# Optimization experiments

Hardware: AMD Instinct MI355X
Metric: run time of the kernel (lower is better)

## Reference

```python
import jax, jax.numpy as jnp
import numpy as np

DIM = 256
NUM_HEADS = 4
HEAD_DIM = DIM // NUM_HEADS
SCALE = HEAD_DIM ** -0.5
LN_EPS = 1e-5


def setup_inputs() -> dict:
    key = jax.random.key(0)
    ks = jax.random.split(key, 12)
    V, B, C, H, W = 3, 2, DIM, 32, 32
    s = 0.02
    return {
        "features": jax.random.normal(ks[0], (V, B, C, H, W), jnp.float32),
        "Wq": jax.random.normal(ks[1], (DIM, DIM), jnp.float32) * s,
        "bq": jnp.zeros((DIM,), jnp.float32),
        "Wk": jax.random.normal(ks[2], (DIM, DIM), jnp.float32) * s,
        "bk": jnp.zeros((DIM,), jnp.float32),
        "Wv": jax.random.normal(ks[3], (DIM, DIM), jnp.float32) * s,
        "bv": jnp.zeros((DIM,), jnp.float32),
        "Wp": jax.random.normal(ks[4], (DIM, DIM), jnp.float32) * s,
        "bp": jnp.zeros((DIM,), jnp.float32),
        "gamma": jnp.ones((DIM,), jnp.float32),
        "beta": jnp.zeros((DIM,), jnp.float32),
    }


def reference(features, Wq, bq, Wk, bk, Wv, bv, Wp, bp, gamma, beta):
    V, B, C, H, W = features.shape
    N = H * W
    L = V * N
    # concat views along token axis: [B, V*N, C]
    x = features.reshape(V, B, C, N).transpose(1, 0, 3, 2).reshape(B, L, C)
    # QKV projections (torch Linear: x @ W.T + b)
    q = (x @ Wq.T + bq).reshape(B, L, NUM_HEADS, HEAD_DIM).transpose(0, 2, 1, 3)
    k = (x @ Wk.T + bk).reshape(B, L, NUM_HEADS, HEAD_DIM).transpose(0, 2, 1, 3)
    v = (x @ Wv.T + bv).reshape(B, L, NUM_HEADS, HEAD_DIM).transpose(0, 2, 1, 3)
    # full attention (chunked loop in original is exact, dropout off in eval)
    attn = jax.nn.softmax(jnp.einsum('bhqd,bhkd->bhqk', q, k) * SCALE, axis=-1)
    o = jnp.einsum('bhqk,bhkd->bhqd', attn, v)  # [B, H, L, D]
    o = o.transpose(0, 2, 1, 3).reshape(B, L, C)
    # output proj + LayerNorm
    o = o @ Wp.T + bp
    mu = jnp.mean(o, axis=-1, keepdims=True)
    var = jnp.mean(jnp.square(o - mu), axis=-1, keepdims=True)
    o = (o - mu) * jax.lax.rsqrt(var + LN_EPS) * gamma + beta
    # mean over views, back to [B, C, H, W]
    o = o.reshape(B, V, N, C).mean(axis=1)
    return o.reshape(B, H, W, C).transpose(0, 3, 1, 2)
```

## Files before the change

### kernel.cpp

```cpp
#include <hip/hip_runtime.h>
#include <hip/hip_bf16.h>

#define V_ 3
#define B_ 2
#define C_ 256
#define N_ 1024
#define L_ 3072
#define NH 4
#define DH 64
#define SCALE 0.125f
#define LOG2E 1.44269504088896340736f

typedef __attribute__((ext_vector_type(8))) short short8;
typedef __attribute__((ext_vector_type(4))) float floatx4;
typedef unsigned short u16;
typedef unsigned int u32;

__device__ __forceinline__ u16 f2bf(float f) {
    union { float f; u32 u; } c; c.f = f;
    u32 u = c.u;
    u32 lsb = (u >> 16) & 1u;
    u += 0x7fffu + lsb;
    return (u16)(u >> 16);
}
__device__ __forceinline__ u32 pk_bf16(float a, float b) {
    __hip_bfloat162 h = __float22bfloat162_rn(make_float2(a, b));
    union { __hip_bfloat162 h; u32 u; } cv; cv.h = h; return cv.u;
}

__global__ __launch_bounds__(256) void k_prep_gather(
    const float* __restrict__ feat,
    const float* __restrict__ Wq, const float* __restrict__ Wk,
    const float* __restrict__ Wv, const float* __restrict__ Wp,
    u16* __restrict__ x, u16* __restrict__ Wb) {
    int bid = blockIdx.x;
    int t = threadIdx.x;
    if (bid < 384) {
        __shared__ u16 tile[64][66];
        int n0 = (bid & 15) << 6;
        int c0 = ((bid >> 4) & 3) << 6;
        int b  = (bid >> 6) & 1;
        int v  = bid >> 7;
        const float* src = feat + ((size_t)((v * B_ + b) * C_ + c0)) * N_ + n0;
        for (int i = 0; i < 8; ++i) {
            int idx = i * 256 + t;
            int cl = idx >> 5;
            int np2 = idx & 31;
            float2 f = *(const float2*)(src + (size_t)cl * N_ + np2 * 2);
            *(u32*)&tile[cl][np2 * 2] = pk_bf16(f.x, f.y);
        }
        __syncthreads();
        u16* dst = x + ((size_t)(b * L_ + v * N_ + n0)) * C_ + c0;
        for (int i = 0; i < 8; ++i) {
            int idx = i * 256 + t;
            int nl = idx >> 5;
            int cl = (idx & 31) * 2;
            u32 uu = (u32)tile[cl][nl] | ((u32)tile[cl + 1][nl] << 16);
            *(u32*)(dst + (size_t)nl * C_ + cl) = uu;
        }
    } else {
        int idx = (bid - 384) * 256 + t;
        int g0 = idx * 16;
        int m = g0 >> 16;
        const float* src = (m == 0) ? Wq : (m == 1) ? Wk : (m == 2) ? Wv : Wp;
        int off = g0 & 65535;
#pragma unroll
        for (int e = 0; e < 8; ++e) {
            float2 f = *(const float2*)(src + off + e * 2);
            ((u32*)(Wb + g0))[e] = pk_bf16(f.x, f.y);
        }
    }
}

__global__ __launch_bounds__(64) void k_qkv(
    const u16* __restrict__ x, const u16* __restrict__ Wb,
    const float* __restrict__ bq, const float* __restrict__ bk,
    const float* __restrict__ bv,
    u16* __restrict__ Qf, u16* __restrict__ Kf, u16* __restrict__ Vf) {
    int bid = blockIdx.x;
    int npc = bid & 3;
    int rest = bid >> 2;
    int m  = rest / 192;
    int rb = rest % 192;
    int b  = rb / 96;
    int r0 = (rb % 96) * 32;
    int lane = threadIdx.x;
    int quad = lane >> 4, m16 = lane & 15;

    const u16* xrow0 = x + ((size_t)(b * L_ + r0 + m16)) * C_ + quad * 8;
    const u16* xrow1 = xrow0 + (size_t)16 * C_;
    short8 a0[8], a1[8];
#pragma unroll
    for (int kc = 0; kc < 8; ++kc) {
        a0[kc] = *(const short8*)(xrow0 + kc * 32);
        a1[kc] = *(const short8*)(xrow1 + kc * 32);
    }
    const u16* W = Wb + (size_t)m * 65536;

    if (m == 2) {
#pragma unroll
        for (int np = npc * 2; np < npc * 2 + 2; ++np) {
            int nt0 = np * 2;
            const u16* w0 = W + (size_t)(nt0 * 16 + m16) * C_ + quad * 8;
            const u16* w1 = w0 + 16 * C_;
            short8 wf0[8], wf1[8];
#pragma unroll
            for (int kc = 0; kc < 8; ++kc) {
                wf0[kc] = *(const short8*)(w0 + kc * 32);
                wf1[kc] = *(const short8*)(w1 + kc * 32);
            }
            floatx4 acc00 = {0.f,0.f,0.f,0.f}, acc01 = {0.f,0.f,0.f,0.f};
            floatx4 acc10 = {0.f,0.f,0.f,0.f}, acc11 = {0.f,0.f,0.f,0.f};
#pragma unroll
            for (int kc = 0; kc < 8; ++kc) {
                acc00 = __builtin_amdgcn_mfma_f32_16x16x32_bf16(a0[kc], wf0[kc], acc00, 0, 0, 0);
                acc01 = __builtin_amdgcn_mfma_f32_16x16x32_bf16(a0[kc], wf1[kc], acc01, 0, 0, 0);
                acc10 = __builtin_amdgcn_mfma_f32_16x16x32_bf16(a1[kc], wf0[kc], acc10, 0, 0, 0);
                acc11 = __builtin_amdgcn_mfma_f32_16x16x32_bf16(a1[kc], wf1[kc], acc11, 0, 0, 0);
            }
#pragma unroll
            for (int gi = 0; gi < 2; ++gi)
#pragma unroll
            for (int half = 0; half < 2; ++half) {
                int dout = (nt0 + half) * 16 + m16;
                float bias = bv[dout];
                int h = dout >> 6, dh = dout & 63;
                size_t bh = (size_t)(b * NH + h);
                floatx4 acc = gi ? (half ? acc11 : acc10) : (half ? acc01 : acc00);
                float f0 = acc[0] + bias, f1 = acc[1] + bias;
                float f2 = acc[2] + bias, f3 = acc[3] + bias;
                int lr0 = r0 + gi * 16 + quad * 4;
                int tile = lr0 >> 6, kk = lr0 & 63;
                int halfv = kk >> 5, quadp = (kk >> 3) & 3, j0 = kk & 7;
                int ntv = dh >> 4, m16pp = dh & 15;
                u32* p = (u32*)(Vf + (bh * 48 + tile) * 4096 +
                                ((size_t)((ntv * 2 + halfv) * 64 + quadp * 16 + m16pp)) * 8 + j0);
                p[0] = pk_bf16(f0, f1);
                p[1] = pk_bf16(f2, f3);
            }
        }
    } else {
        const float* bs = (m == 0) ? bq : bk;
        float scale = (m == 0) ? (SCALE * LOG2E) : 1.0f;
#pragma unroll
        for (int np = npc * 2; np < npc * 2 + 2; ++np) {
            int nt0 = np * 2;
            const u16* w0 = W + (size_t)(nt0 * 16 + m16) * C_ + quad * 8;
            const u16* w1 = w0 + 16 * C_;
            short8 wf0[8], wf1[8];
#pragma unroll
            for (int kc = 0; kc < 8; ++kc) {
                wf0[kc] = *(const short8*)(w0 + kc * 32);
                wf1[kc] = *(const short8*)(w1 + kc * 32);
            }
            floatx4 acc00 = {0.f,0.f,0.f,0.f}, acc01 = {0.f,0.f,0.f,0.f};
            floatx4 acc10 = {0.f,0.f,0.f,0.f}, acc11 = {0.f,0.f,0.f,0.f};
#pragma unroll
            for (int kc = 0; kc < 8; ++kc) {
                acc00 = __builtin_amdgcn_mfma_f32_16x16x32_bf16(wf0[kc], a0[kc], acc00, 0, 0, 0);
                acc01 = __builtin_amdgcn_mfma_f32_16x16x32_bf16(wf0[kc], a1[kc], acc01, 0, 0, 0);
                acc10 = __builtin_amdgcn_mfma_f32_16x16x32_bf16(wf1[kc], a0[kc], acc10, 0, 0, 0);
                acc11 = __builtin_amdgcn_mfma_f32_16x16x32_bf16(wf1[kc], a1[kc], acc11, 0, 0, 0);
            }
#pragma unroll
            for (int tt = 0; tt < 2; ++tt)
#pragma unroll
            for (int gi = 0; gi < 2; ++gi) {
                int ntb = (nt0 + tt) * 16;
                int h = ntb >> 6;
                size_t bh = (size_t)(b * NH + h);
                int dh0 = (ntb & 63) + quad * 4;
                int cc = dh0 >> 5, qp = (dh0 >> 3) & 3, j0 = dh0 & 7;
                float4 b4 = *(const float4*)(bs + ntb + quad * 4);
                floatx4 acc = tt ? (gi ? acc11 : acc10) : (gi ? acc01 : acc00);
                float f0 = (acc[0] + b4.x) * scale, f1 = (acc[1] + b4.y) * scale;
                float f2 = (acc[2] + b4.z) * scale, f3 = (acc[3] + b4.w) * scale;
                uint2 pk;
                pk.x = pk_bf16(f0, f1);
                pk.y = pk_bf16(f2, f3);
                int token = r0 + gi * 16 + m16;
                if (m == 0) {
                    int grp = (r0 >> 4) + gi;
                    *(uint2*)(Qf + (bh * 192 + grp) * 1024 +
                              (size_t)(cc * 64 + qp * 16 + m16) * 8 + j0) = pk;
                } else {
                    int tile = token >> 6;
                    int ntk = ((r0 & 63) >> 4) + gi;
                    *(uint2*)(Kf + (bh * 48 + tile) * 4096 +
                              (size_t)((ntk * 2 + cc) * 64 + qp * 16 + m16) * 8 + j0) = pk;
                }
            }
        }
    }
}

__global__ __launch_bounds__(256, 2) void k_attn(
    const u16* __restrict__ Qf, const u16* __restrict__ Kf,
    const u16* __restrict__ Vf, u16* __restrict__ o) {
    __shared__ __align__(16) char smem[55296];
    __shared__ float l_red[3][3][16];
    u16* PL = (u16*)smem;
    float* o_red = (float*)smem;
    int bid = blockIdx.x;
    int qt = bid & 63;
    int h  = (bid >> 6) & 3;
    int b  = bid >> 8;
    int lane = threadIdx.x & 63;
    int w    = threadIdx.x >> 6;
    int quad = lane >> 4, m16 = lane & 15;
    int q0 = qt * 48;
    size_t bh = (size_t)(b * NH + h);

    const u16* qbase = Qf + (bh * 192 + qt * 3) * 1024 + (size_t)lane * 8;
    const u16* kbase = Kf + bh * 48 * 4096 + (size_t)lane * 8;
    const u16* vbase = Vf + bh * 48 * 4096 + (size_t)lane * 8;

    short8 aq[3][2];
#pragma unroll
    for (int g = 0; g < 3; ++g) {
        aq[g][0] = *(const short8*)(qbase + g * 1024);
        aq[g][1] = *(const short8*)(qbase + g * 1024 + 512);
    }

    float l_s[3] = {0.f, 0.f, 0.f};
    floatx4 o_acc[3][4];
#pragma unroll
    for (int g = 0; g < 3; ++g)
#pragma unroll
        for (int nt = 0; nt < 4; ++nt) o_acc[g][nt] = (floatx4){0.f, 0.f, 0.f, 0.f};

    int kt0 = w * 12;
    short8 kb[8], vb[8];

#pragma unroll
    for (int f = 0; f < 8; ++f)
        kb[f] = *(const short8*)(kbase + (size_t)kt0 * 4096 + f * 512);
#pragma unroll
    for (int g = 0; g < 3; ++g) {
        floatx4 sx[4];
#pragma unroll
        for (int nt = 0; nt < 4; ++nt) {
            floatx4 z = {0.f, 0.f, 0.f, 0.f};
            z = __builtin_amdgcn_mfma_f32_16x16x32_bf16(kb[nt * 2], aq[g][0], z, 0, 0, 0);
            sx[nt] = __builtin_amdgcn_mfma_f32_16x16x32_bf16(kb[nt * 2 + 1], aq[g][1], z, 0, 0, 0);
        }
        u16* plrow = PL + ((0 * 12 + w * 3 + g) * 16 + m16) * 72;
        float lsum = 0.f;
#pragma unroll
        for (int nt = 0; nt < 4; ++nt) {
            float p0 = __builtin_amdgcn_exp2f(sx[nt][0]);
            float p1 = __builtin_amdgcn_exp2f(sx[nt][1]);
            float p2 = __builtin_amdgcn_exp2f(sx[nt][2]);
            float p3 = __builtin_amdgcn_exp2f(sx[nt][3]);
            lsum += (p0 + p1) + (p2 + p3);
            uint2 pk; pk.x = pk_bf16(p0, p1); pk.y = pk_bf16(p2, p3);
            *(uint2*)(plrow + nt * 16 + quad * 4) = pk;
        }
        l_s[g] += lsum;
    }

    for (int i = 0; i < 12; ++i) {
        int cur = i & 1, nxt = cur ^ 1;
        size_t tbase = (size_t)(kt0 + i) * 4096;
#pragma unroll
        for (int f = 0; f < 8; ++f)
            vb[f] = *(const short8*)(vbase + tbase + f * 512);
        short8 bp[3][2];
#pragma unroll
        for (int g = 0; g < 3; ++g) {
            const u16* plrow = PL + ((cur * 12 + w * 3 + g) * 16 + m16) * 72;
            bp[g][0] = *(const short8*)(plrow + quad * 8);
            bp[g][1] = *(const short8*)(plrow + 32 + quad * 8);
        }
        if (i < 11) {
#pragma unroll
            for (int f = 0; f < 8; ++f)
                kb[f] = *(const short8*)(kbase + tbase + 4096 + f * 512);
        }
#pragma unroll
        for (int g = 0; g < 3; ++g)
#pragma unroll
            for (int nt = 0; nt < 4; ++nt) {
                o_acc[g][nt] = __builtin_amdgcn_mfma_f32_16x16x32_bf16(vb[nt * 2], bp[g][0], o_acc[g][nt], 0, 0, 0);
                o_acc[g][nt] = __builtin_amdgcn_mfma_f32_16x16x32_bf16(vb[nt * 2 + 1], bp[g][1], o_acc[g][nt], 0, 0, 0);
            }
        if (i < 11) {
#pragma unroll
            for (int g = 0; g < 3; ++g) {
                floatx4 sx[4];
#pragma unroll
                for (int nt = 0; nt < 4; ++nt) {
                    floatx4 z = {0.f, 0.f, 0.f, 0.f};
                    z = __builtin_amdgcn_mfma_f32_16x16x32_bf16(kb[nt * 2], aq[g][0], z, 0, 0, 0);
                    sx[nt] = __builtin_amdgcn_mfma_f32_16x16x32_bf16(kb[nt * 2 + 1], aq[g][1], z, 0, 0, 0);
                }
                u16* plrow = PL + ((nxt * 12 + w * 3 + g) * 16 + m16) * 72;
                float lsum = 0.f;
#pragma unroll
                for (int nt = 0; nt < 4; ++nt) {
                    float p0 = __builtin_amdgcn_exp2f(sx[nt][0]);
                    float p1 = __builtin_amdgcn_exp2f(sx[nt][1]);
                    float p2 = __builtin_amdgcn_exp2f(sx[nt][2]);
                    float p3 = __builtin_amdgcn_exp2f(sx[nt][3]);
                    lsum += (p0 + p1) + (p2 + p3);
                    uint2 pk; pk.x = pk_bf16(p0, p1); pk.y = pk_bf16(p2, p3);
                    *(uint2*)(plrow + nt * 16 + quad * 4) = pk;
                }
                l_s[g] += lsum;
            }
        }
    }
    float l_row[3];
#pragma unroll
    for (int g = 0; g < 3; ++g) {
        float ps = l_s[g];
        ps += __shfl_xor(ps, 16);
        ps += __shfl_xor(ps, 32);
        l_row[g] = ps;
    }
    __syncthreads();
    if (w > 0) {
#pragma unroll
        for (int g = 0; g < 3; ++g) {
#pragma unroll
            for (int nt = 0; nt < 4; ++nt)
                *(floatx4*)&o_red[(((w - 1) * 3 + g) * 4 + nt) * 256 + lane * 4] = o_acc[g][nt];
            if (quad == 0) l_red[w - 1][g][m16] = l_row[g];
        }
    }
    __syncthreads();
    if (w == 0) {
#pragma unroll
        for (int g = 0; g < 3; ++g) {
            float lt = __builtin_amdgcn_rcpf(
                l_row[g] + l_red[0][g][m16] + l_red[1][g][m16] + l_red[2][g][m16]);
#pragma unroll
            for (int nt = 0; nt < 4; ++nt) {
                floatx4 tot = o_acc[g][nt];
#pragma unroll
                for (int w1 = 0; w1 < 3; ++w1)
                    tot += *(const floatx4*)&o_red[((w1 * 3 + g) * 4 + nt) * 256 + lane * 4];
                uint2 pk;
                pk.x = pk_bf16(tot[0] * lt, tot[1] * lt);
                pk.y = pk_bf16(tot[2] * lt, tot[3] * lt);
                *(uint2*)(o + ((size_t)(b * L_ + q0 + g * 16 + m16)) * C_ +
                          h * 64 + nt * 16 + quad * 4) = pk;
            }
        }
    }
}

__global__ __launch_bounds__(256) void k_proj_ln(
    const u16* __restrict__ o, const u16* __restrict__ Wpb,
    const float* __restrict__ bp,
    const float* __restrict__ gamma, const float* __restrict__ beta,
    u16* __restrict__ oln) {
    __shared__ float sred[4][16];
    __shared__ float sred2[4][16];
    int bid = blockIdx.x;
    int n0 = (bid & 63) << 4;
    int b  = (bid >> 6) & 1;
    int v  = bid >> 7;
    int lane = threadIdx.x & 63;
    int w    = threadIdx.x >> 6;
    int quad = lane >> 4, m16 = lane & 15;

    const u16* orow = o + ((size_t)(b * L_ + v * N_ + n0 + m16)) * C_ + quad * 8;
    short8 a[8];
#pragma unroll
    for (int kc = 0; kc < 8; ++kc) a[kc] = *(const short8*)(orow + kc * 32);

    float pr[4][4];
#pragma unroll
    for (int j = 0; j < 4; ++j) {
        int nt = w * 4 + j;
        const u16* wrow = Wpb + (size_t)(nt * 16 + m16) * C_ + quad * 8;
        floatx4 acc = {0.f, 0.f, 0.f, 0.f};
#pragma unroll
        for (int kc = 0; kc < 8; ++kc) {
            short8 bfr = *(const short8*)(wrow + kc * 32);
            acc = __builtin_amdgcn_mfma_f32_16x16x32_bf16(bfr, a[kc], acc, 0, 0, 0);
        }
        float4 b4 = *(const float4*)(bp + nt * 16 + quad * 4);
        pr[j][0] = acc[0] + b4.x; pr[j][1] = acc[1] + b4.y;
        pr[j][2] = acc[2] + b4.z; pr[j][3] = acc[3] + b4.w;
    }
    float sm = 0.f;
#pragma unroll
    for (int j = 0; j < 4; ++j)
        sm += (pr[j][0] + pr[j][1]) + (pr[j][2] + pr[j][3]);
    sm += __shfl_xor(sm, 16);
    sm += __shfl_xor(sm, 32);
    if (quad == 0) sred[w][m16] = sm;
    __syncthreads();
    float mu = (sred[0][m16] + sred[1][m16] + sred[2][m16] + sred[3][m16]) * (1.0f / C_);
    float sq = 0.f;
#pragma unroll
    for (int j = 0; j < 4; ++j)
#pragma unroll
        for (int r = 0; r < 4; ++r) { float d = pr[j][r] - mu; sq += d * d; }
    sq += __shfl_xor(sq, 16);
    sq += __shfl_xor(sq, 32);
    if (quad == 0) sred2[w][m16] = sq;
    __syncthreads();
    float var = (sred2[0][m16] + sred2[1][m16] + sred2[2][m16] + sred2[3][m16]) * (1.0f / C_);
    float rs = __builtin_amdgcn_rsqf(var + 1e-5f);
#pragma unroll
    for (int j = 0; j < 4; ++j) {
        int c0 = (w * 4 + j) * 16 + quad * 4;
        float4 g4 = *(const float4*)(gamma + c0);
        float4 be4 = *(const float4*)(beta + c0);
        float f0 = (pr[j][0] - mu) * rs * g4.x + be4.x;
        float f1 = (pr[j][1] - mu) * rs * g4.y + be4.y;
        float f2 = (pr[j][2] - mu) * rs * g4.z + be4.z;
        float f3 = (pr[j][3] - mu) * rs * g4.w + be4.w;
        uint2 pk;
        pk.x = pk_bf16(f0, f1);
        pk.y = pk_bf16(f2, f3);
        *(uint2*)(oln + ((size_t)((v * B_ + b) * N_ + n0 + m16)) * C_ + c0) = pk;
    }
}

__global__ __launch_bounds__(256) void k_mean_t(
    const u16* __restrict__ oln, float* __restrict__ out) {
    __shared__ float tile[64][65];
    int bid = blockIdx.x;
    int n0 = (bid & 15) << 6;
    int c0 = ((bid >> 4) & 3) << 6;
    int b  = bid >> 6;
    int t = threadIdx.x;
    union { u32 u; float f; } cv;
    for (int i = 0; i < 16; ++i) {
        int idx = i * 256 + t;
        int nl = idx >> 6, cl = idx & 63;
        float sm = 0.f;
#pragma unroll
        for (int v = 0; v < 3; ++v) {
            u16 raw = oln[((size_t)((v * B_ + b) * N_ + n0 + nl)) * C_ + c0 + cl];
            cv.u = ((u32)raw) << 16;
            sm += cv.f;
        }
        tile[cl][nl] = sm * (1.0f / 3.0f);
    }
    __syncthreads();
    for (int i = 0; i < 16; ++i) {
        int idx = i * 256 + t;
        int cl = idx >> 6, nl = idx & 63;
        out[((size_t)(b * C_ + c0 + cl)) * N_ + n0 + nl] = tile[cl][nl];
    }
}

extern "C" void kernel_launch(void* const* d_in, const int* in_sizes, int n_in,
                              void* d_out, int out_size, void* d_ws, size_t ws_size,
                              hipStream_t stream) {
    (void)in_sizes; (void)n_in; (void)out_size; (void)ws_size;
    const float* feat  = (const float*)d_in[0];
    const float* Wq    = (const float*)d_in[1];
    const float* bq    = (const float*)d_in[2];
    const float* Wk    = (const float*)d_in[3];
    const float* bk    = (const float*)d_in[4];
    const float* Wv    = (const float*)d_in[5];
    const float* bv    = (const float*)d_in[6];
    const float* Wp    = (const float*)d_in[7];
    const float* bp    = (const float*)d_in[8];
    const float* gamma = (const float*)d_in[9];
    const float* beta  = (const float*)d_in[10];
    float* out = (float*)d_out;

    size_t SZ = (size_t)B_ * L_ * C_;
    u16* x   = (u16*)d_ws;
    u16* Qf  = x + SZ;
    u16* Kf  = Qf + SZ;
    u16* Vf  = Kf + SZ;
    u16* o   = Vf + SZ;
    u16* Wb  = o + SZ;
    u16* oln = Wb + 4 * 65536;

    k_prep_gather<<<dim3(448), dim3(256), 0, stream>>>(feat, Wq, Wk, Wv, Wp, x, Wb);
    k_qkv<<<dim3(2304), dim3(64), 0, stream>>>(x, Wb, bq, bk, bv, Qf, Kf, Vf);
    k_attn<<<dim3(512), dim3(256), 0, stream>>>(Qf, Kf, Vf, o);
    k_proj_ln<<<dim3(384), dim3(256), 0, stream>>>(o, Wb + 3 * 65536, bp, gamma, beta, oln);
    k_mean_t<<<dim3(128), dim3(256), 0, stream>>>(oln, out);
}
```

Baseline: 137.3 us.

## Fuse view-mean into LayerNorm via atomics and simplify attention P buffering

Removes the separate mean/transpose kernel and intermediate bf16 buffer: the output is zeroed in the prep kernel and the LayerNorm epilogue atomically accumulates one third of each view's result directly into the transposed output. The attention loop drops its double-buffered score/PV software pipeline in favour of computing scores, softmax and PV per group sequentially, shrinking shared memory. This saves a launch and a global round trip, but adds strided atomic traffic and loses the overlap of the score MFMAs with the PV MFMAs.

```diff
diff --git a/kernel.cpp b/kernel.cpp
--- a/kernel.cpp
+++ b/kernel.cpp
@@ -16,13 +16,6 @@
 typedef unsigned short u16;
 typedef unsigned int u32;
 
-__device__ __forceinline__ u16 f2bf(float f) {
-    union { float f; u32 u; } c; c.f = f;
-    u32 u = c.u;
-    u32 lsb = (u >> 16) & 1u;
-    u += 0x7fffu + lsb;
-    return (u16)(u >> 16);
-}
 __device__ __forceinline__ u32 pk_bf16(float a, float b) {
     __hip_bfloat162 h = __float22bfloat162_rn(make_float2(a, b));
     union { __hip_bfloat162 h; u32 u; } cv; cv.h = h; return cv.u;
@@ -32,7 +25,7 @@
     const float* __restrict__ feat,
     const float* __restrict__ Wq, const float* __restrict__ Wk,
     const float* __restrict__ Wv, const float* __restrict__ Wp,
-    u16* __restrict__ x, u16* __restrict__ Wb) {
+    u16* __restrict__ x, u16* __restrict__ Wb, float* __restrict__ out) {
     int bid = blockIdx.x;
     int t = threadIdx.x;
     if (bid < 384) {
@@ -58,7 +51,7 @@
             u32 uu = (u32)tile[cl][nl] | ((u32)tile[cl + 1][nl] << 16);
             *(u32*)(dst + (size_t)nl * C_ + cl) = uu;
         }
-    } else {
+    } else if (bid < 448) {
         int idx = (bid - 384) * 256 + t;
         int g0 = idx * 16;
         int m = g0 >> 16;
@@ -69,6 +62,12 @@
             float2 f = *(const float2*)(src + off + e * 2);
             ((u32*)(Wb + g0))[e] = pk_bf16(f.x, f.y);
         }
+    } else {
+        size_t g0 = ((size_t)(bid - 448) * 256 + t) * 16;
+        float4 z = {0.f, 0.f, 0.f, 0.f};
+#pragma unroll
+        for (int e = 0; e < 4; ++e)
+            *(float4*)(out + g0 + e * 4) = z;
     }
 }
 
@@ -197,7 +196,7 @@
 __global__ __launch_bounds__(256, 2) void k_attn(
     const u16* __restrict__ Qf, const u16* __restrict__ Kf,
     const u16* __restrict__ Vf, u16* __restrict__ o) {
-    __shared__ __align__(16) char smem[55296];
+    __shared__ __align__(16) char smem[36864];
     __shared__ float l_red[3][3][16];
     u16* PL = (u16*)smem;
     float* o_red = (float*)smem;
@@ -231,83 +230,49 @@
 
     int kt0 = w * 12;
     short8 kb[8], vb[8];
-
 #pragma unroll
     for (int f = 0; f < 8; ++f)
         kb[f] = *(const short8*)(kbase + (size_t)kt0 * 4096 + f * 512);
-#pragma unroll
-    for (int g = 0; g < 3; ++g) {
-        floatx4 sx[4];
-#pragma unroll
-        for (int nt = 0; nt < 4; ++nt) {
-            floatx4 z = {0.f, 0.f, 0.f, 0.f};
-            z = __builtin_amdgcn_mfma_f32_16x16x32_bf16(kb[nt * 2], aq[g][0], z, 0, 0, 0);
-            sx[nt] = __builtin_amdgcn_mfma_f32_16x16x32_bf16(kb[nt * 2 + 1], aq[g][1], z, 0, 0, 0);
-        }
-        u16* plrow = PL + ((0 * 12 + w * 3 + g) * 16 + m16) * 72;
-        float lsum = 0.f;
-#pragma unroll
-        for (int nt = 0; nt < 4; ++nt) {
-            float p0 = __builtin_amdgcn_exp2f(sx[nt][0]);
-            float p1 = __builtin_amdgcn_exp2f(sx[nt][1]);
-            float p2 = __builtin_amdgcn_exp2f(sx[nt][2]);
-            float p3 = __builtin_amdgcn_exp2f(sx[nt][3]);
-            lsum += (p0 + p1) + (p2 + p3);
-            uint2 pk; pk.x = pk_bf16(p0, p1); pk.y = pk_bf16(p2, p3);
-            *(uint2*)(plrow + nt * 16 + quad * 4) = pk;
-        }
-        l_s[g] += lsum;
-    }
 
     for (int i = 0; i < 12; ++i) {
-        int cur = i & 1, nxt = cur ^ 1;
         size_t tbase = (size_t)(kt0 + i) * 4096;
 #pragma unroll
         for (int f = 0; f < 8; ++f)
             vb[f] = *(const short8*)(vbase + tbase + f * 512);
-        short8 bp[3][2];
 #pragma unroll
         for (int g = 0; g < 3; ++g) {
-            const u16* plrow = PL + ((cur * 12 + w * 3 + g) * 16 + m16) * 72;
-            bp[g][0] = *(const short8*)(plrow + quad * 8);
-            bp[g][1] = *(const short8*)(plrow + 32 + quad * 8);
+            floatx4 sx[4];
+#pragma unroll
+            for (int nt = 0; nt < 4; ++nt) {
+                floatx4 z = {0.f, 0.f, 0.f, 0.f};
+                z = __builtin_amdgcn_mfma_f32_16x16x32_bf16(kb[nt * 2], aq[g][0], z, 0, 0, 0);
+                sx[nt] = __builtin_amdgcn_mfma_f32_16x16x32_bf16(kb[nt * 2 + 1], aq[g][1], z, 0, 0, 0);
+            }
+            u16* plrow = PL + (((w * 3 + g) * 16) + m16) * 72;
+            float lsum = 0.f;
+#pragma unroll
+            for (int nt = 0; nt < 4; ++nt) {
+                float p0 = __builtin_amdgcn_exp2f(sx[nt][0]);
+                float p1 = __builtin_amdgcn_exp2f(sx[nt][1]);
+                float p2 = __builtin_amdgcn_exp2f(sx[nt][2]);
+                float p3 = __builtin_amdgcn_exp2f(sx[nt][3]);
+                lsum += (p0 + p1) + (p2 + p3);
+                uint2 pk; pk.x = pk_bf16(p0, p1); pk.y = pk_bf16(p2, p3);
+                *(uint2*)(plrow + nt * 16 + quad * 4) = pk;
+            }
+            l_s[g] += lsum;
+            short8 bp0 = *(const short8*)(plrow + quad * 8);
+            short8 bp1 = *(const short8*)(plrow + 32 + quad * 8);
+#pragma unroll
+            for (int nt = 0; nt < 4; ++nt) {
+                o_acc[g][nt] = __builtin_amdgcn_mfma_f32_16x16x32_bf16(vb[nt * 2], bp0, o_acc[g][nt], 0, 0, 0);
+                o_acc[g][nt] = __builtin_amdgcn_mfma_f32_16x16x32_bf16(vb[nt * 2 + 1], bp1, o_acc[g][nt], 0, 0, 0);
+            }
         }
         if (i < 11) {
 #pragma unroll
             for (int f = 0; f < 8; ++f)
                 kb[f] = *(const short8*)(kbase + tbase + 4096 + f * 512);
-        }
-#pragma unroll
-        for (int g = 0; g < 3; ++g)
-#pragma unroll
-            for (int nt = 0; nt < 4; ++nt) {
-                o_acc[g][nt] = __builtin_amdgcn_mfma_f32_16x16x32_bf16(vb[nt * 2], bp[g][0], o_acc[g][nt], 0, 0, 0);
-                o_acc[g][nt] = __builtin_amdgcn_mfma_f32_16x16x32_bf16(vb[nt * 2 + 1], bp[g][1], o_acc[g][nt], 0, 0, 0);
-            }
-        if (i < 11) {
-#pragma unroll
-            for (int g = 0; g < 3; ++g) {
-                floatx4 sx[4];
-#pragma unroll
-                for (int nt = 0; nt < 4; ++nt) {
-                    floatx4 z = {0.f, 0.f, 0.f, 0.f};
-                    z = __builtin_amdgcn_mfma_f32_16x16x32_bf16(kb[nt * 2], aq[g][0], z, 0, 0, 0);
-                    sx[nt] = __builtin_amdgcn_mfma_f32_16x16x32_bf16(kb[nt * 2 + 1], aq[g][1], z, 0, 0, 0);
-                }
-                u16* plrow = PL + ((nxt * 12 + w * 3 + g) * 16 + m16) * 72;
-                float lsum = 0.f;
-#pragma unroll
-                for (int nt = 0; nt < 4; ++nt) {
-                    float p0 = __builtin_amdgcn_exp2f(sx[nt][0]);
-                    float p1 = __builtin_amdgcn_exp2f(sx[nt][1]);
-                    float p2 = __builtin_amdgcn_exp2f(sx[nt][2]);
-                    float p3 = __builtin_amdgcn_exp2f(sx[nt][3]);
-                    lsum += (p0 + p1) + (p2 + p3);
-                    uint2 pk; pk.x = pk_bf16(p0, p1); pk.y = pk_bf16(p2, p3);
-                    *(uint2*)(plrow + nt * 16 + quad * 4) = pk;
-                }
-                l_s[g] += lsum;
-            }
         }
     }
     float l_row[3];
@@ -354,7 +319,7 @@
     const u16* __restrict__ o, const u16* __restrict__ Wpb,
     const float* __restrict__ bp,
     const float* __restrict__ gamma, const float* __restrict__ beta,
-    u16* __restrict__ oln) {
+    float* __restrict__ out) {
     __shared__ float sred[4][16];
     __shared__ float sred2[4][16];
     int bid = blockIdx.x;
@@ -405,48 +370,17 @@
     __syncthreads();
     float var = (sred2[0][m16] + sred2[1][m16] + sred2[2][m16] + sred2[3][m16]) * (1.0f / C_);
     float rs = __builtin_amdgcn_rsqf(var + 1e-5f);
+    int n = n0 + m16;
 #pragma unroll
     for (int j = 0; j < 4; ++j) {
         int c0 = (w * 4 + j) * 16 + quad * 4;
         float4 g4 = *(const float4*)(gamma + c0);
         float4 be4 = *(const float4*)(beta + c0);
-        float f0 = (pr[j][0] - mu) * rs * g4.x + be4.x;
-        float f1 = (pr[j][1] - mu) * rs * g4.y + be4.y;
-        float f2 = (pr[j][2] - mu) * rs * g4.z + be4.z;
-        float f3 = (pr[j][3] - mu) * rs * g4.w + be4.w;
-        uint2 pk;
-        pk.x = pk_bf16(f0, f1);
-        pk.y = pk_bf16(f2, f3);
-        *(uint2*)(oln + ((size_t)((v * B_ + b) * N_ + n0 + m16)) * C_ + c0) = pk;
-    }
-}
-
-__global__ __launch_bounds__(256) void k_mean_t(
-    const u16* __restrict__ oln, float* __restrict__ out) {
-    __shared__ float tile[64][65];
-    int bid = blockIdx.x;
-    int n0 = (bid & 15) << 6;
-    int c0 = ((bid >> 4) & 3) << 6;
-    int b  = bid >> 6;
-    int t = threadIdx.x;
-    union { u32 u; float f; } cv;
-    for (int i = 0; i < 16; ++i) {
-        int idx = i * 256 + t;
-        int nl = idx >> 6, cl = idx & 63;
-        float sm = 0.f;
-#pragma unroll
-        for (int v = 0; v < 3; ++v) {
-            u16 raw = oln[((size_t)((v * B_ + b) * N_ + n0 + nl)) * C_ + c0 + cl];
-            cv.u = ((u32)raw) << 16;
-            sm += cv.f;
-        }
-        tile[cl][nl] = sm * (1.0f / 3.0f);
-    }
-    __syncthreads();
-    for (int i = 0; i < 16; ++i) {
-        int idx = i * 256 + t;
-        int cl = idx >> 6, nl = idx & 63;
-        out[((size_t)(b * C_ + c0 + cl)) * N_ + n0 + nl] = tile[cl][nl];
+        float* obase = out + ((size_t)(b * C_ + c0)) * N_ + n;
+        atomicAdd(obase,          ((pr[j][0] - mu) * rs * g4.x + be4.x) * (1.0f / 3.0f));
+        atomicAdd(obase + N_,     ((pr[j][1] - mu) * rs * g4.y + be4.y) * (1.0f / 3.0f));
+        atomicAdd(obase + 2 * N_, ((pr[j][2] - mu) * rs * g4.z + be4.z) * (1.0f / 3.0f));
+        atomicAdd(obase + 3 * N_, ((pr[j][3] - mu) * rs * g4.w + be4.w) * (1.0f / 3.0f));
     }
 }
 
@@ -474,11 +408,9 @@
     u16* Vf  = Kf + SZ;
     u16* o   = Vf + SZ;
     u16* Wb  = o + SZ;
-    u16* oln = Wb + 4 * 65536;
-
-    k_prep_gather<<<dim3(448), dim3(256), 0, stream>>>(feat, Wq, Wk, Wv, Wp, x, Wb);
+
+    k_prep_gather<<<dim3(576), dim3(256), 0, stream>>>(feat, Wq, Wk, Wv, Wp, x, Wb, out);
     k_qkv<<<dim3(2304), dim3(64), 0, stream>>>(x, Wb, bq, bk, bv, Qf, Kf, Vf);
     k_attn<<<dim3(512), dim3(256), 0, stream>>>(Qf, Kf, Vf, o);
-    k_proj_ln<<<dim3(384), dim3(256), 0, stream>>>(o, Wb + 3 * 65536, bp, gamma, beta, oln);
-    k_mean_t<<<dim3(128), dim3(256), 0, stream>>>(oln, out);
-}
+    k_proj_ln<<<dim3(384), dim3(256), 0, stream>>>(o, Wb + 3 * 65536, bp, gamma, beta, out);
+}
```

New measurement: 132.8 us. 1.03x faster.
